# Performance work log

Hardware: AMD Instinct MI355X
Metric: run time of the kernel (lower is better)

The kernel has to match this reference:

```python
import jax, jax.numpy as jnp
import numpy as np

B, T, C = 2, 2048, 1024
H = 16
HD = C // H  # 64
BLOCK_SIZE = 2048
ROPE_BASE = 10000.0
NEG_INF = float('-inf')


def setup_inputs() -> dict:
    key = jax.random.key(0)
    k1, k2, k3, k4, k5, k6, k7 = jax.random.split(key, 7)
    x = jax.random.normal(k1, (B, T, C), dtype=jnp.float32)
    cumulative_scores = jax.random.normal(k2, (B, T), dtype=jnp.float32)
    padding_mask = jnp.ones((B, BLOCK_SIZE), dtype=jnp.bool_)
    token_index = jax.random.randint(k3, (B, T), 0, BLOCK_SIZE, dtype=jnp.int32)
    c_attn_weight = 0.02 * jax.random.normal(k4, (C, 3 * C), dtype=jnp.float32)
    c_attn_bias = jnp.zeros((3 * C,), dtype=jnp.float32)
    c_proj_weight = 0.02 * jax.random.normal(k5, (C, C), dtype=jnp.float32)
    c_proj_bias = jnp.zeros((C,), dtype=jnp.float32)
    return {
        'x': x,
        'cumulative_scores': cumulative_scores,
        'padding_mask': padding_mask,
        'token_index': token_index,
        'c_attn_weight': c_attn_weight,
        'c_attn_bias': c_attn_bias,
        'c_proj_weight': c_proj_weight,
        'c_proj_bias': c_proj_bias,
    }


def _rotate_half(x):
    x1, x2 = x[..., : x.shape[-1] // 2], x[..., x.shape[-1] // 2:]
    return jnp.concatenate((-x2, x1), axis=-1)


def _forward(x, cumulative_scores, c_attn_weight, c_attn_bias, c_proj_weight,
             c_proj_bias, token_index, padding_mask):
    # qkv projection
    qkv = x @ c_attn_weight + c_attn_bias
    q, k, v = jnp.split(qkv, 3, axis=2)
    q = q.reshape(B, T, H, HD).transpose(0, 2, 1, 3)  # [B,H,T,HD]
    k = k.reshape(B, T, H, HD).transpose(0, 2, 1, 3)
    v = v.reshape(B, T, H, HD).transpose(0, 2, 1, 3)

    # data-dependent per-token rotation amounts (faithful to source: the
    # scatter x.at[..., idx].add(1) with 2D idx accumulates over all batches)
    token_counts = jnp.zeros((B, BLOCK_SIZE), dtype=token_index.dtype)
    token_counts = token_counts.at[..., token_index].add(1)
    inv_counts = 1.0 / (token_counts + 1e-10)  # [B, BLOCK_SIZE] float32
    partial_rotations = jnp.cumsum(
        jnp.take_along_axis(inv_counts, token_index, axis=-1), axis=-1)  # [B,T]

    # RoPE with per-token t
    inv_freq = 1.0 / ROPE_BASE ** (jnp.arange(0, HD, 2, dtype=jnp.float32) / HD)
    freqs = jnp.einsum('bt,j->btj', partial_rotations, inv_freq)  # [B,T,HD/2]
    emb = jnp.concatenate((freqs, freqs), axis=-1)  # [B,T,HD]
    cos = jnp.cos(emb)[:, None, :, :]  # [B,1,T,HD]
    sin = jnp.sin(emb)[:, None, :, :]
    q = q * cos + _rotate_half(q) * sin
    k = k * cos + _rotate_half(k) * sin

    # fork plan: overwrite last channel of q with ones, of k with cum scores
    q = q.at[:, :, :, -1].set(1.0)
    k = k.at[:, :, :, -1].set(jnp.broadcast_to(cumulative_scores[:, None, :], (B, H, T)))

    # causal + padding additive mask
    causal = jnp.where(jnp.tril(jnp.ones((T, T), dtype=jnp.bool_)), 0.0, NEG_INF)  # [T,T]
    pm = jnp.take_along_axis(padding_mask, token_index, axis=1).astype(jnp.float32)  # [B,T]
    pm_outer = pm[:, :, None] * pm[:, None, :]  # [B,T,T]
    pm_add = jnp.where(pm_outer.astype(jnp.bool_), 0.0, NEG_INF)
    mask = causal[None, :, :] + pm_add  # [B,T,T]

    # v scaled by exp(cumulative_scores) along L
    v = v * jnp.exp(cumulative_scores)[:, None, :, None]

    scale = 1.0 / jnp.sqrt(jnp.asarray(HD, dtype=jnp.float32))
    attn = jnp.einsum('bnqd,bnkd->bnqk', q, k) * scale + mask[:, None, :, :]
    attn = jax.nn.softmax(attn, axis=-1)
    y = jnp.einsum('bnqk,bnkd->bnqd', attn, v)
    y = y.transpose(0, 2, 1, 3).reshape(B, T, C)
    return y @ c_proj_weight + c_proj_bias


def reference(x, cumulative_scores, padding_mask, token_index, c_attn_weight,
              c_attn_bias, c_proj_weight, c_proj_bias):
    return _forward(x, cumulative_scores, c_attn_weight, c_attn_bias,
                    c_proj_weight, c_proj_bias, token_index, padding_mask)
```

## Files before the change

### kernel.cpp

```cpp
#include <hip/hip_runtime.h>
#include <hip/hip_bf16.h>
#include <math.h>

#define Bb 2
#define Tt 2048
#define Cc 1024
#define Hh 16
#define HDd 64
#define QSCALE 0.18033688011112042f

typedef __attribute__((ext_vector_type(8))) short short8;
typedef __attribute__((ext_vector_type(4))) short short4v;
typedef __attribute__((ext_vector_type(4))) float f32x4;

#if defined(__has_builtin)
#if __has_builtin(__builtin_amdgcn_global_load_lds)
#define USE_GLL 1
#endif
#endif
#define AS_GLOBAL __attribute__((address_space(1)))
#define AS_LDS    __attribute__((address_space(3)))

__device__ __forceinline__ float bf2f(unsigned short u){
  union { unsigned int i; float f; } v; v.i = ((unsigned int)u)<<16; return v.f;
}
__device__ __forceinline__ unsigned short f2bf(float f){
  union { float f; unsigned int i; } v; v.f = f;
  unsigned int x = v.i;
  return (unsigned short)((x + 0x7fffu + ((x>>16)&1u)) >> 16);
}
__device__ __forceinline__ unsigned int cvtpk_bf16(float lo, float hi){
  unsigned int r;
  asm("v_cvt_pk_bf16_f32 %0, %1, %2" : "=v"(r) : "v"(lo), "v"(hi));
  return r;
}
__device__ __forceinline__ float exp2fast(float x){
  float r; asm("v_exp_f32 %0, %1" : "=v"(r) : "v"(x)); return r;
}
__device__ __forceinline__ f32x4 mfma16(short4v a, short4v b, f32x4 c){
#if defined(__has_builtin)
#if __has_builtin(__builtin_amdgcn_mfma_f32_16x16x16_bf16)
  return __builtin_amdgcn_mfma_f32_16x16x16_bf16(a, b, c, 0, 0, 0);
#elif __has_builtin(__builtin_amdgcn_mfma_f32_16x16x16bf16_1k)
  return __builtin_amdgcn_mfma_f32_16x16x16bf16_1k(a, b, c, 0, 0, 0);
#else
  asm("v_mfma_f32_16x16x16_bf16 %0, %1, %2, %3" : "=v"(c) : "v"(a), "v"(b), "0"(c));
  return c;
#endif
#else
  asm("v_mfma_f32_16x16x16_bf16 %0, %1, %2, %3" : "=v"(c) : "v"(a), "v"(b), "0"(c));
  return c;
#endif
}

__global__ __launch_bounds__(256) void k_f2b(const float* __restrict__ in,
                                             unsigned short* __restrict__ out, int n){
  int i = (blockIdx.x*256 + threadIdx.x)*8;
  if (i >= n) return;
  float4 v0 = *(const float4*)(in + i);
  float4 v1 = *(const float4*)(in + i + 4);
  union { unsigned int u[4]; int4 v; } pk;
  pk.u[0] = cvtpk_bf16(v0.x, v0.y);
  pk.u[1] = cvtpk_bf16(v0.z, v0.w);
  pk.u[2] = cvtpk_bf16(v1.x, v1.y);
  pk.u[3] = cvtpk_bf16(v1.z, v1.w);
  *(int4*)(out + i) = pk.v;
}

__global__ __launch_bounds__(256) void k_transpose_f2b(const float* __restrict__ w0,
                                                       const float* __restrict__ w1,
                                                       unsigned short* __restrict__ o0,
                                                       unsigned short* __restrict__ o1){
  __shared__ float tile[32][33];
  const int K = 1024;
  int which = blockIdx.z;
  const float* in = which ? w1 : w0;
  unsigned short* out = which ? o1 : o0;
  int N = which ? 1024 : 3072;
  if (blockIdx.x*32 >= N) return;
  int kb = blockIdx.y*32, nb = blockIdx.x*32;
  int tx = threadIdx.x, ty = threadIdx.y;
  #pragma unroll
  for (int i=0;i<4;i++)
    tile[ty+i*8][tx] = in[(size_t)(kb+ty+i*8)*N + nb + tx];
  __syncthreads();
  #pragma unroll
  for (int i=0;i<4;i++)
    out[(size_t)(nb+ty+i*8)*K + kb + tx] = f2bf(tile[tx][ty+i*8]);
}

__global__ __launch_bounds__(1024) void k_scan(const int* __restrict__ tok,
                                               float* __restrict__ cs_t){
  __shared__ int cnt[2048];
  __shared__ float vals[2048];
  __shared__ float psum[1024];
  int b = blockIdx.x;
  int tid = threadIdx.x;
  cnt[tid] = 0; cnt[tid+1024] = 0;
  __syncthreads();
  for (int i = tid; i < Bb*Tt; i += 1024) atomicAdd(&cnt[tok[i]], 1);
  __syncthreads();
  for (int i = tid; i < Tt; i += 1024){
    int idx = tok[b*Tt + i];
    vals[i] = 1.0f / ((float)cnt[idx] + 1e-10f);
  }
  __syncthreads();
  float s0 = vals[2*tid], s1 = vals[2*tid+1];
  psum[tid] = s0 + s1;
  __syncthreads();
  for (int off=1; off<1024; off<<=1){
    float add = (tid>=off) ? psum[tid-off] : 0.0f;
    __syncthreads();
    psum[tid] += add;
    __syncthreads();
  }
  float base = (tid>0) ? psum[tid-1] : 0.0f;
  vals[2*tid]   = base + s0;
  vals[2*tid+1] = base + s0 + s1;
  __syncthreads();
  for (int i = tid; i < Tt*32; i += 1024){
    int t = i >> 5, j = i & 31;
    float invf = exp2f(-(float)j * 0.4152410118609203f);
    float ang = vals[t] * invf;
    float2 cs = make_float2(cosf(ang), sinf(ang));
    *(float2*)&cs_t[((size_t)b*Tt + t)*64 + 2*j] = cs;
  }
}

__global__ __launch_bounds__(256, 4) void k_gemmQKV(const unsigned short* __restrict__ A,
                                                    const unsigned short* __restrict__ Bt,
                                                    const float* __restrict__ bias,
                                                    const float* __restrict__ cs_t,
                                                    const float* __restrict__ cum,
                                                    unsigned short* __restrict__ Qo,
                                                    unsigned short* __restrict__ Ko,
                                                    unsigned short* __restrict__ VTo){
  __shared__ union {
    unsigned short ab[2][128][64];
    unsigned short vb[32][140];
  } sm;
  const int K = 1024, N = 3072;
  int mb = blockIdx.y*128, nb = blockIdx.x*128;
  int tid = threadIdx.x;
  int wave = tid>>6, lane = tid&63;
  int wr = wave>>1, wc = wave&1;
  int lrow = lane&15, lhi = lane>>4;
  f32x4 acc[4][4] = {};
  int r0 = tid>>3;
  int g0 = tid&7;
  int gsw = (g0 ^ (r0&7)) << 3;
  const unsigned short* Asrc = A  + (size_t)(mb + r0)*K + gsw;
  const unsigned short* Bsrc = Bt + (size_t)(nb + r0)*K + gsw;
  const size_t rstep = (size_t)32*K;
#ifdef USE_GLL
  for (int kb=0; kb<K; kb+=64){
    #pragma unroll
    for (int i=0;i<4;i++){
      __builtin_amdgcn_global_load_lds((const AS_GLOBAL void*)(Asrc + i*rstep + kb),
                                       (AS_LDS void*)&sm.ab[0][r0+32*i][g0*8], 16, 0, 0);
      __builtin_amdgcn_global_load_lds((const AS_GLOBAL void*)(Bsrc + i*rstep + kb),
                                       (AS_LDS void*)&sm.ab[1][r0+32*i][g0*8], 16, 0, 0);
    }
    __syncthreads();
    #pragma unroll
    for (int ks=0; ks<2; ks++){
      short8 af[4], bf[4];
      #pragma unroll
      for (int m=0;m<4;m++){
        int R = 64*wr + 16*m + lrow;
        af[m] = *(const short8*)&sm.ab[0][R][((4*ks+lhi)^(R&7))<<3];
      }
      #pragma unroll
      for (int n=0;n<4;n++){
        int R = 64*wc + 16*n + lrow;
        bf[n] = *(const short8*)&sm.ab[1][R][((4*ks+lhi)^(R&7))<<3];
      }
      #pragma unroll
      for (int m=0;m<4;m++)
        #pragma unroll
        for (int n=0;n<4;n++)
          acc[m][n] = __builtin_amdgcn_mfma_f32_16x16x32_bf16(af[m], bf[n], acc[m][n], 0,0,0);
    }
    __syncthreads();
  }
#else
  for (int kb=0; kb<K; kb+=64){
    int4 st[8];
    #pragma unroll
    for (int i=0;i<4;i++){
      st[2*i]   = *(const int4*)(Asrc + i*rstep + kb);
      st[2*i+1] = *(const int4*)(Bsrc + i*rstep + kb);
    }
    __syncthreads();
    #pragma unroll
    for (int i=0;i<4;i++){
      *(int4*)&sm.ab[0][r0+32*i][g0*8] = st[2*i];
      *(int4*)&sm.ab[1][r0+32*i][g0*8] = st[2*i+1];
    }
    __syncthreads();
    #pragma unroll
    for (int ks=0; ks<2; ks++){
      short8 af[4], bf[4];
      #pragma unroll
      for (int m=0;m<4;m++){
        int R = 64*wr + 16*m + lrow;
        af[m] = *(const short8*)&sm.ab[0][R][((4*ks+lhi)^(R&7))<<3];
      }
      #pragma unroll
      for (int n=0;n<4;n++){
        int R = 64*wc + 16*n + lrow;
        bf[n] = *(const short8*)&sm.ab[1][R][((4*ks+lhi)^(R&7))<<3];
      }
      #pragma unroll
      for (int m=0;m<4;m++)
        #pragma unroll
        for (int n=0;n<4;n++)
          acc[m][n] = __builtin_amdgcn_mfma_f32_16x16x32_bf16(af[m], bf[n], acc[m][n], 0,0,0);
    }
    __syncthreads();
  }
#endif
  int type = nb >> 10;
  int h0 = (nb >> 6) & 15;
  int h  = h0 + wc;
  int b_ = mb >> 11;
  int tb_ = mb & 2047;
  float bz[4];
  #pragma unroll
  for (int n=0;n<4;n++) bz[n] = bias[nb + 64*wc + 16*n + lrow];

  if (type < 2){
    unsigned short* dst = (type==0) ? Qo : Ko;
    #pragma unroll
    for (int m=0;m<4;m++)
      #pragma unroll
      for (int q=0;q<4;q++){
        int rl = 64*wr + 16*m + 4*lhi + q;
        int row = mb + rl;
        float2 cs0 = *(const float2*)&cs_t[(size_t)row*64 + 2*lrow];
        float2 cs1 = *(const float2*)&cs_t[(size_t)row*64 + 32 + 2*lrow];
        float a0 = acc[m][0][q] + bz[0];
        float a1 = acc[m][1][q] + bz[1];
        float a2 = acc[m][2][q] + bz[2];
        float a3 = acc[m][3][q] + bz[3];
        float r0v = a0*cs0.x - a2*cs0.y;
        float r1v = a1*cs1.x - a3*cs1.y;
        float r2v = a2*cs0.x + a0*cs0.y;
        float r3v = a3*cs1.x + a1*cs1.y;
        if (type==0){
          if (lrow==15) r3v = 1.0f;
          r0v *= QSCALE; r1v *= QSCALE; r2v *= QSCALE; r3v *= QSCALE;
        } else {
          if (lrow==15) r3v = cum[row];
        }
        size_t base = (((size_t)b_*Hh + h)*Tt + (row & 2047))*HDd + lrow;
        dst[base]      = f2bf(r0v);
        dst[base + 16] = f2bf(r1v);
        dst[base + 32] = f2bf(r2v);
        dst[base + 48] = f2bf(r3v);
      }
  } else {
    for (int pass=0; pass<4; pass++){
      __syncthreads();
      if (wr == (pass>>1)){
        int m0 = 2*(pass&1);
        #pragma unroll
        for (int mm=0; mm<2; mm++){
          int m = m0 + mm;
          #pragma unroll
          for (int q=0;q<4;q++){
            int rl32 = 16*mm + 4*lhi + q;
            float vs = __expf(cum[mb + 32*pass + rl32]);
            sm.vb[rl32][64*wc + lrow]      = f2bf((acc[m][0][q]+bz[0])*vs);
            sm.vb[rl32][64*wc + 16+lrow]   = f2bf((acc[m][1][q]+bz[1])*vs);
            sm.vb[rl32][64*wc + 32+lrow]   = f2bf((acc[m][2][q]+bz[2])*vs);
            sm.vb[rl32][64*wc + 48+lrow]   = f2bf((acc[m][3][q]+bz[3])*vs);
          }
        }
      }
      __syncthreads();
      #pragma unroll
      for (int i=0;i<16;i++){
        int idx = i*256 + tid;
        int t_l = idx & 31;
        int dh  = idx >> 5;
        int d   = dh & 63;
        int hh  = dh >> 6;
        VTo[(((size_t)b_*Hh + h0 + hh)*HDd + d)*Tt + tb_ + 32*pass + t_l] = sm.vb[t_l][64*hh + d];
      }
    }
  }
}

__global__ __launch_bounds__(256) void k_gemm64(const unsigned short* __restrict__ A,
                                                const unsigned short* __restrict__ Bt,
                                                const float* __restrict__ bias,
                                                float* __restrict__ Cout,
                                                int M, int N, int K){
  __shared__ unsigned short As[64][32];
  __shared__ unsigned short Bs[128][32];
  int mb = blockIdx.y*64, nb = blockIdx.x*128;
  int tid = threadIdx.x;
  int wave = tid>>6, lane = tid&63;
  int wr = wave>>1, wc = wave&1;
  int lrow = lane&15, lhi = lane>>4;
  f32x4 acc[2][4] = {};
  int r0 = tid>>2;
  int gd = tid&3;
  int gs0 = (gd ^ ((r0>>1)&3)) << 3;
  const unsigned short* Arow  = A  + (size_t)(mb + r0)*K      + gs0;
  const unsigned short* Brow0 = Bt + (size_t)(nb + r0)*K      + gs0;
  const unsigned short* Brow1 = Bt + (size_t)(nb + r0 + 64)*K + gs0;
#ifdef USE_GLL
  for (int kb=0; kb<K; kb+=32){
    __builtin_amdgcn_global_load_lds((const AS_GLOBAL void*)(Arow + kb),
                                     (AS_LDS void*)&As[r0][gd*8],    16, 0, 0);
    __builtin_amdgcn_global_load_lds((const AS_GLOBAL void*)(Brow0 + kb),
                                     (AS_LDS void*)&Bs[r0][gd*8],    16, 0, 0);
    __builtin_amdgcn_global_load_lds((const AS_GLOBAL void*)(Brow1 + kb),
                                     (AS_LDS void*)&Bs[r0+64][gd*8], 16, 0, 0);
    __syncthreads();
    short8 af[2], bf[4];
    #pragma unroll
    for (int m=0;m<2;m++){
      int R = 32*wr + 16*m + lrow;
      af[m] = *(const short8*)&As[R][(lhi^((R>>1)&3))<<3];
    }
    #pragma unroll
    for (int n=0;n<4;n++){
      int R = 64*wc + 16*n + lrow;
      bf[n] = *(const short8*)&Bs[R][(lhi^((R>>1)&3))<<3];
    }
    #pragma unroll
    for (int m=0;m<2;m++)
      #pragma unroll
      for (int n=0;n<4;n++)
        acc[m][n] = __builtin_amdgcn_mfma_f32_16x16x32_bf16(af[m], bf[n], acc[m][n], 0,0,0);
    __syncthreads();
  }
#else
  for (int kb=0; kb<K; kb+=32){
    int4 a0 = *(const int4*)(Arow + kb);
    int4 b0 = *(const int4*)(Brow0 + kb);
    int4 b1 = *(const int4*)(Brow1 + kb);
    __syncthreads();
    *(int4*)&As[r0][gd*8]    = a0;
    *(int4*)&Bs[r0][gd*8]    = b0;
    *(int4*)&Bs[r0+64][gd*8] = b1;
    __syncthreads();
    short8 af[2], bf[4];
    #pragma unroll
    for (int m=0;m<2;m++){
      int R = 32*wr + 16*m + lrow;
      af[m] = *(const short8*)&As[R][(lhi^((R>>1)&3))<<3];
    }
    #pragma unroll
    for (int n=0;n<4;n++){
      int R = 64*wc + 16*n + lrow;
      bf[n] = *(const short8*)&Bs[R][(lhi^((R>>1)&3))<<3];
    }
    #pragma unroll
    for (int m=0;m<2;m++)
      #pragma unroll
      for (int n=0;n<4;n++)
        acc[m][n] = __builtin_amdgcn_mfma_f32_16x16x32_bf16(af[m], bf[n], acc[m][n], 0,0,0);
  }
#endif
  #pragma unroll
  for (int m=0;m<2;m++)
    #pragma unroll
    for (int n=0;n<4;n++)
      #pragma unroll
      for (int q=0;q<4;q++){
        int row = mb + 32*wr + 16*m + 4*lhi + q;
        int col = nb + 64*wc + 16*n + lrow;
        Cout[(size_t)row*N + col] = acc[m][n][q] + bias[col];
      }
}

__global__ __launch_bounds__(512, 4) void k_attn8(const unsigned short* __restrict__ Q,
                                                  const unsigned short* __restrict__ K,
                                                  const unsigned short* __restrict__ VT,
                                                  unsigned short* __restrict__ Y){
  __shared__ __align__(16) char smem[65536];
  typedef unsigned short (*tile_t)[2][4096];
  tile_t Ks = (tile_t)smem;
  tile_t Vs = (tile_t)(smem + 32768);
  float (*cmb)[64][35] = (float (*)[64][35])smem;

  int bh = blockIdx.y; int b = bh >> 4, h = bh & 15;
  int s_ = blockIdx.x;
  int tid = threadIdx.x;
  int wave = tid>>6, lane = tid&63;
  int wpair = wave & 3, p = wave >> 2;
  int lrow = lane&15, lhi = lane>>4;
  const unsigned short* Qh = Q + (((size_t)b*Hh + h)*Tt)*HDd;
  const unsigned short* Kh = K + (((size_t)b*Hh + h)*Tt)*HDd;
  const unsigned short* Vh = VT + (((size_t)b*Hh + h)*HDd)*Tt;
  int qL0 = 64*s_ + 16*wpair;
  int qH0 = 1984 - 64*s_ + 16*wpair;
  short8 qfL0 = *(const short8*)&Qh[(size_t)(qL0+lrow)*HDd + 8*lhi];
  short8 qfL1 = *(const short8*)&Qh[(size_t)(qL0+lrow)*HDd + 32 + 8*lhi];
  short8 qfH0 = *(const short8*)&Qh[(size_t)(qH0+lrow)*HDd + 8*lhi];
  short8 qfH1 = *(const short8*)&Qh[(size_t)(qH0+lrow)*HDd + 32 + 8*lhi];
  f32x4 oL[4] = {}, oH[4] = {};
  float lsL = 0.0f, lsH = 0.0f;
  int rowL = qL0 + lrow, rowH = qH0 + lrow;
  int ntL = s_ + 1;
  int NTH = 32 - s_;
  int NI  = (NTH + 1) >> 1;

  int kr = tid >> 3, kc = tid & 7;
  int o_ = tid * 16;
  int ksrc = kr*HDd + ((kc ^ (kr&7)) << 3);
  int vsrc = kr*Tt  + ((kc ^ (kr&7)) << 3);

#ifdef USE_GLL
#define STAGE2(bufi, base_) do { \
    __builtin_amdgcn_global_load_lds((const AS_GLOBAL void*)(Kh + (size_t)(base_)*64*HDd + ksrc), \
        (AS_LDS void*)((AS_LDS char*)&Ks[bufi][0][0] + o_), 16, 0, 0); \
    __builtin_amdgcn_global_load_lds((const AS_GLOBAL void*)(Vh + (size_t)(base_)*64 + vsrc), \
        (AS_LDS void*)((AS_LDS char*)&Vs[bufi][0][0] + o_), 16, 0, 0); \
    if ((base_)+1 < NTH){ \
      __builtin_amdgcn_global_load_lds((const AS_GLOBAL void*)(Kh + (size_t)((base_)+1)*64*HDd + ksrc), \
          (AS_LDS void*)((AS_LDS char*)&Ks[bufi][1][0] + o_), 16, 0, 0); \
      __builtin_amdgcn_global_load_lds((const AS_GLOBAL void*)(Vh + (size_t)((base_)+1)*64 + vsrc), \
          (AS_LDS void*)((AS_LDS char*)&Vs[bufi][1][0] + o_), 16, 0, 0); \
    } \
  } while(0)
#else
#define STAGE2(bufi, base_) do { \
    int4 a_ = *(const int4*)(Kh + (size_t)(base_)*64*HDd + ksrc); \
    int4 c_ = *(const int4*)(Vh + (size_t)(base_)*64 + vsrc); \
    *(int4*)((char*)&Ks[bufi][0][0] + o_) = a_; \
    *(int4*)((char*)&Vs[bufi][0][0] + o_) = c_; \
    if ((base_)+1 < NTH){ \
      int4 b_ = *(const int4*)(Kh + (size_t)((base_)+1)*64*HDd + ksrc); \
      int4 d_ = *(const int4*)(Vh + (size_t)((base_)+1)*64 + vsrc); \
      *(int4*)((char*)&Ks[bufi][1][0] + o_) = b_; \
      *(int4*)((char*)&Vs[bufi][1][0] + o_) = d_; \
    } \
  } while(0)
#endif

  STAGE2(0, 0);
  int buf = 0;
  for (int i = 0; i < NI; i++){
    __syncthreads();
    if (i+1 < NI) STAGE2(buf^1, 2*(i+1));
    int kt = 2*i + p;
    if (kt < NTH){
      int k0 = kt*64;
      bool doL = (kt < ntL);
      const unsigned short* Kbase = &Ks[buf][p][0];
      const unsigned short* Vbase = &Vs[buf][p][0];
      f32x4 sL[4] = {}, sH[4] = {};
      __builtin_amdgcn_s_setprio(1);
      #pragma unroll
      for (int j=0;j<4;j++){
        int krow = 16*j + lrow;
        #pragma unroll
        for (int ks=0;ks<2;ks++){
          int dgrp = (4*ks + lhi) ^ (krow&7);
          short8 kf = *(const short8*)&Kbase[krow*64 + dgrp*8];
          sH[j] = __builtin_amdgcn_mfma_f32_16x16x32_bf16(kf, ks ? qfH1 : qfH0, sH[j], 0,0,0);
          if (doL) sL[j] = __builtin_amdgcn_mfma_f32_16x16x32_bf16(kf, ks ? qfL1 : qfL0, sL[j], 0,0,0);
        }
      }
      __builtin_amdgcn_s_setprio(0);
      short4v paH[4], paL[4];
      {
        bool diagH = (k0 + 63 >= qH0);
        #pragma unroll
        for (int j=0;j<4;j++){
          int kbase = k0 + 16*j + 4*lhi;
          float p0 = exp2fast(sH[j][0]);
          float p1 = exp2fast(sH[j][1]);
          float p2 = exp2fast(sH[j][2]);
          float p3 = exp2fast(sH[j][3]);
          if (diagH){
            if (kbase + 0 > rowH) p0 = 0.0f;
            if (kbase + 1 > rowH) p1 = 0.0f;
            if (kbase + 2 > rowH) p2 = 0.0f;
            if (kbase + 3 > rowH) p3 = 0.0f;
          }
          lsH += (p0 + p1) + (p2 + p3);
          union { unsigned int u[2]; short4v v; } pk;
          pk.u[0] = cvtpk_bf16(p0, p1);
          pk.u[1] = cvtpk_bf16(p2, p3);
          paH[j] = pk.v;
        }
      }
      if (doL){
        bool diagL = (k0 + 63 >= qL0);
        #pragma unroll
        for (int j=0;j<4;j++){
          int kbase = k0 + 16*j + 4*lhi;
          float p0 = exp2fast(sL[j][0]);
          float p1 = exp2fast(sL[j][1]);
          float p2 = exp2fast(sL[j][2]);
          float p3 = exp2fast(sL[j][3]);
          if (diagL){
            if (kbase + 0 > rowL) p0 = 0.0f;
            if (kbase + 1 > rowL) p1 = 0.0f;
            if (kbase + 2 > rowL) p2 = 0.0f;
            if (kbase + 3 > rowL) p3 = 0.0f;
          }
          lsL += (p0 + p1) + (p2 + p3);
          union { unsigned int u[2]; short4v v; } pk;
          pk.u[0] = cvtpk_bf16(p0, p1);
          pk.u[1] = cvtpk_bf16(p2, p3);
          paL[j] = pk.v;
        }
      }
      __builtin_amdgcn_s_setprio(1);
      #pragma unroll
      for (int jp=0;jp<4;jp++){
        int vrow = 16*jp + lrow;
        #pragma unroll
        for (int j=0;j<4;j++){
          int byte_in_row = ((((2*j + (lhi>>1)) ^ (vrow&7)) << 4) | ((lhi&1) << 3));
          short4v vf = *(const short4v*)((const char*)&Vbase[vrow*64] + byte_in_row);
          oH[jp] = mfma16(vf, paH[j], oH[jp]);
          if (doL) oL[jp] = mfma16(vf, paL[j], oL[jp]);
        }
      }
      __builtin_amdgcn_s_setprio(0);
    }
    buf ^= 1;
  }

  __syncthreads();
  if (p == 1){
    float* c = &cmb[wpair][lane][0];
    #pragma unroll
    for (int jp=0;jp<4;jp++)
      #pragma unroll
      for (int r=0;r<4;r++){
        c[4*jp+r]    = oL[jp][r];
        c[16+4*jp+r] = oH[jp][r];
      }
    c[32] = lsL; c[33] = lsH;
  }
  __syncthreads();
  if (p == 0){
    const float* c = &cmb[wpair][lane][0];
    #pragma unroll
    for (int jp=0;jp<4;jp++)
      #pragma unroll
      for (int r=0;r<4;r++){
        oL[jp][r] += c[4*jp+r];
        oH[jp][r] += c[16+4*jp+r];
      }
    lsL += c[32]; lsH += c[33];
    lsL += __shfl_xor(lsL, 16); lsL += __shfl_xor(lsL, 32);
    lsH += __shfl_xor(lsH, 16); lsH += __shfl_xor(lsH, 32);
    float invL = 1.0f / lsL, invH = 1.0f / lsH;
    size_t rbL = ((size_t)b*Tt + qL0 + lrow)*Cc + h*HDd + 4*lhi;
    size_t rbH = ((size_t)b*Tt + qH0 + lrow)*Cc + h*HDd + 4*lhi;
    #pragma unroll
    for (int jp=0;jp<4;jp++){
      unsigned int l0 = cvtpk_bf16(oL[jp][0]*invL, oL[jp][1]*invL);
      unsigned int l1 = cvtpk_bf16(oL[jp][2]*invL, oL[jp][3]*invL);
      unsigned int h0_ = cvtpk_bf16(oH[jp][0]*invH, oH[jp][1]*invH);
      unsigned int h1_ = cvtpk_bf16(oH[jp][2]*invH, oH[jp][3]*invH);
      *(unsigned long long*)&Y[rbL + 16*jp] = (unsigned long long)l0 | ((unsigned long long)l1<<32);
      *(unsigned long long*)&Y[rbH + 16*jp] = (unsigned long long)h0_ | ((unsigned long long)h1_<<32);
    }
  }
#undef STAGE2
}

extern "C" void kernel_launch(void* const* d_in, const int* in_sizes, int n_in,
                              void* d_out, int out_size, void* d_ws, size_t ws_size,
                              hipStream_t stream){
  const float* x     = (const float*)d_in[0];
  const float* cum   = (const float*)d_in[1];
  const int*   tok   = (const int*)d_in[3];
  const float* Wqkv  = (const float*)d_in[4];
  const float* bqkv  = (const float*)d_in[5];
  const float* Wproj = (const float*)d_in[6];
  const float* bproj = (const float*)d_in[7];

  char* ws = (char*)d_ws;
  size_t off = 0;
  auto alloc = [&](size_t bytes)->void*{
    void* p = ws + off; off += (bytes + 255) & ~(size_t)255; return p;
  };
  unsigned short* wqkvT = (unsigned short*)alloc((size_t)3072*1024*2);
  unsigned short* wprojT= (unsigned short*)alloc((size_t)1024*1024*2);
  unsigned short* xb    = (unsigned short*)alloc((size_t)4096*1024*2);
  unsigned short* Qb    = (unsigned short*)alloc((size_t)Bb*Hh*Tt*HDd*2);
  unsigned short* Kb    = (unsigned short*)alloc((size_t)Bb*Hh*Tt*HDd*2);
  unsigned short* VTb   = (unsigned short*)alloc((size_t)Bb*Hh*Tt*HDd*2);
  float* cs_t           = (float*)alloc((size_t)Bb*Tt*64*4);
  unsigned short* Y     = xb;

  k_f2b<<<dim3(4096*1024/8/256), dim3(256), 0, stream>>>(x, xb, 4096*1024);
  k_transpose_f2b<<<dim3(3072/32, 1024/32, 2), dim3(32,8), 0, stream>>>(Wqkv, Wproj, wqkvT, wprojT);
  k_scan<<<dim3(Bb), dim3(1024), 0, stream>>>(tok, cs_t);
  k_gemmQKV<<<dim3(3072/128, 4096/128), dim3(256), 0, stream>>>(xb, wqkvT, bqkv, cs_t, cum, Qb, Kb, VTb);
  k_attn8<<<dim3(16, Bb*Hh), dim3(512), 0, stream>>>(Qb, Kb, VTb, Y);
  k_gemm64<<<dim3(1024/128, 4096/64), dim3(256), 0, stream>>>(Y, wprojT, bproj, (float*)d_out, 4096, 1024, 1024);
}
```

Baseline: 133.7 us.

## Fuse fp32-to-bf16 conversion of x into the QKV GEMM A-tile load

Removes the separate k_f2b conversion kernel and has the QKV GEMM load fp32 activations straight into LDS with an XOR swizzle, converting to bf16 when building the MFMA fragments. This saves one launch plus a full write and read of the bf16 copy of x. In exchange the A tile in LDS doubles in size (fp32), which may lower occupancy, and the conversion is repeated by every N-column block. It also raises wave priority around the MFMA loop with s_setprio.

```diff
diff --git a/kernel.cpp b/kernel.cpp
--- a/kernel.cpp
+++ b/kernel.cpp
@@ -51,20 +51,6 @@
   asm("v_mfma_f32_16x16x16_bf16 %0, %1, %2, %3" : "=v"(c) : "v"(a), "v"(b), "0"(c));
   return c;
 #endif
-}
-
-__global__ __launch_bounds__(256) void k_f2b(const float* __restrict__ in,
-                                             unsigned short* __restrict__ out, int n){
-  int i = (blockIdx.x*256 + threadIdx.x)*8;
-  if (i >= n) return;
-  float4 v0 = *(const float4*)(in + i);
-  float4 v1 = *(const float4*)(in + i + 4);
-  union { unsigned int u[4]; int4 v; } pk;
-  pk.u[0] = cvtpk_bf16(v0.x, v0.y);
-  pk.u[1] = cvtpk_bf16(v0.z, v0.w);
-  pk.u[2] = cvtpk_bf16(v1.x, v1.y);
-  pk.u[3] = cvtpk_bf16(v1.z, v1.w);
-  *(int4*)(out + i) = pk.v;
 }
 
 __global__ __launch_bounds__(256) void k_transpose_f2b(const float* __restrict__ w0,
@@ -127,7 +113,7 @@
   }
 }
 
-__global__ __launch_bounds__(256, 4) void k_gemmQKV(const unsigned short* __restrict__ A,
+__global__ __launch_bounds__(256, 4) void k_gemmQKV(const float* __restrict__ A,
                                                     const unsigned short* __restrict__ Bt,
                                                     const float* __restrict__ bias,
                                                     const float* __restrict__ cs_t,
@@ -136,7 +122,10 @@
                                                     unsigned short* __restrict__ Ko,
                                                     unsigned short* __restrict__ VTo){
   __shared__ union {
-    unsigned short ab[2][128][64];
+    struct {
+      float          Af[128][64];
+      unsigned short Bs[128][64];
+    } s;
     unsigned short vb[32][140];
   } sm;
   const int K = 1024, N = 3072;
@@ -146,20 +135,26 @@
   int wr = wave>>1, wc = wave&1;
   int lrow = lane&15, lhi = lane>>4;
   f32x4 acc[4][4] = {};
-  int r0 = tid>>3;
-  int g0 = tid&7;
-  int gsw = (g0 ^ (r0&7)) << 3;
-  const unsigned short* Asrc = A  + (size_t)(mb + r0)*K + gsw;
-  const unsigned short* Bsrc = Bt + (size_t)(nb + r0)*K + gsw;
-  const size_t rstep = (size_t)32*K;
+  int r0b = tid>>3, g0 = tid&7;
+  int gswB = (g0 ^ (r0b&7)) << 3;
+  const unsigned short* Bsrc = Bt + (size_t)(nb + r0b)*K + gswB;
+  const size_t rstepB = (size_t)32*K;
+  int ar = tid>>1;
 #ifdef USE_GLL
   for (int kb=0; kb<K; kb+=64){
     #pragma unroll
+    for (int i=0;i<8;i++){
+      int flat = i*256 + tid;
+      int r = flat >> 4, g = flat & 15;
+      __builtin_amdgcn_global_load_lds(
+        (const AS_GLOBAL void*)(A + (size_t)(mb + r)*K + kb + ((g ^ (r&7)) << 2)),
+        (AS_LDS void*)&sm.s.Af[r][g<<2], 16, 0, 0);
+    }
+    #pragma unroll
     for (int i=0;i<4;i++){
-      __builtin_amdgcn_global_load_lds((const AS_GLOBAL void*)(Asrc + i*rstep + kb),
-                                       (AS_LDS void*)&sm.ab[0][r0+32*i][g0*8], 16, 0, 0);
-      __builtin_amdgcn_global_load_lds((const AS_GLOBAL void*)(Bsrc + i*rstep + kb),
-                                       (AS_LDS void*)&sm.ab[1][r0+32*i][g0*8], 16, 0, 0);
+      __builtin_amdgcn_global_load_lds(
+        (const AS_GLOBAL void*)(Bsrc + i*rstepB + kb),
+        (AS_LDS void*)&sm.s.Bs[r0b+32*i][g0*8], 16, 0, 0);
     }
     __syncthreads();
     #pragma unroll
@@ -168,35 +163,51 @@
       #pragma unroll
       for (int m=0;m<4;m++){
         int R = 64*wr + 16*m + lrow;
-        af[m] = *(const short8*)&sm.ab[0][R][((4*ks+lhi)^(R&7))<<3];
+        int G0 = 8*ks + 2*lhi;
+        f32x4 a0 = *(const f32x4*)&sm.s.Af[R][(G0     ^ (R&7)) << 2];
+        f32x4 a1 = *(const f32x4*)&sm.s.Af[R][((G0+1) ^ (R&7)) << 2];
+        union { unsigned int u[4]; short8 v; } pa;
+        pa.u[0] = cvtpk_bf16(a0[0], a0[1]);
+        pa.u[1] = cvtpk_bf16(a0[2], a0[3]);
+        pa.u[2] = cvtpk_bf16(a1[0], a1[1]);
+        pa.u[3] = cvtpk_bf16(a1[2], a1[3]);
+        af[m] = pa.v;
       }
       #pragma unroll
       for (int n=0;n<4;n++){
         int R = 64*wc + 16*n + lrow;
-        bf[n] = *(const short8*)&sm.ab[1][R][((4*ks+lhi)^(R&7))<<3];
-      }
+        bf[n] = *(const short8*)&sm.s.Bs[R][((4*ks+lhi)^(R&7))<<3];
+      }
+      __builtin_amdgcn_s_setprio(1);
       #pragma unroll
       for (int m=0;m<4;m++)
         #pragma unroll
         for (int n=0;n<4;n++)
           acc[m][n] = __builtin_amdgcn_mfma_f32_16x16x32_bf16(af[m], bf[n], acc[m][n], 0,0,0);
+      __builtin_amdgcn_s_setprio(0);
     }
     __syncthreads();
   }
 #else
   for (int kb=0; kb<K; kb+=64){
-    int4 st[8];
-    #pragma unroll
-    for (int i=0;i<4;i++){
-      st[2*i]   = *(const int4*)(Asrc + i*rstep + kb);
-      st[2*i+1] = *(const int4*)(Bsrc + i*rstep + kb);
-    }
-    __syncthreads();
-    #pragma unroll
-    for (int i=0;i<4;i++){
-      *(int4*)&sm.ab[0][r0+32*i][g0*8] = st[2*i];
-      *(int4*)&sm.ab[1][r0+32*i][g0*8] = st[2*i+1];
-    }
+    float4 sa[8]; int4 sb[4];
+    #pragma unroll
+    for (int i=0;i<8;i++){
+      int flat = i*256 + tid;
+      int r = flat >> 4, g = flat & 15;
+      sa[i] = *(const float4*)(A + (size_t)(mb + r)*K + kb + ((g ^ (r&7)) << 2));
+    }
+    #pragma unroll
+    for (int i=0;i<4;i++) sb[i] = *(const int4*)(Bsrc + i*rstepB + kb);
+    __syncthreads();
+    #pragma unroll
+    for (int i=0;i<8;i++){
+      int flat = i*256 + tid;
+      int r = flat >> 4, g = flat & 15;
+      *(float4*)&sm.s.Af[r][g<<2] = sa[i];
+    }
+    #pragma unroll
+    for (int i=0;i<4;i++) *(int4*)&sm.s.Bs[r0b+32*i][g0*8] = sb[i];
     __syncthreads();
     #pragma unroll
     for (int ks=0; ks<2; ks++){
@@ -204,12 +215,20 @@
       #pragma unroll
       for (int m=0;m<4;m++){
         int R = 64*wr + 16*m + lrow;
-        af[m] = *(const short8*)&sm.ab[0][R][((4*ks+lhi)^(R&7))<<3];
+        int G0 = 8*ks + 2*lhi;
+        f32x4 a0 = *(const f32x4*)&sm.s.Af[R][(G0     ^ (R&7)) << 2];
+        f32x4 a1 = *(const f32x4*)&sm.s.Af[R][((G0+1) ^ (R&7)) << 2];
+        union { unsigned int u[4]; short8 v; } pa;
+        pa.u[0] = cvtpk_bf16(a0[0], a0[1]);
+        pa.u[1] = cvtpk_bf16(a0[2], a0[3]);
+        pa.u[2] = cvtpk_bf16(a1[0], a1[1]);
+        pa.u[3] = cvtpk_bf16(a1[2], a1[3]);
+        af[m] = pa.v;
       }
       #pragma unroll
       for (int n=0;n<4;n++){
         int R = 64*wc + 16*n + lrow;
-        bf[n] = *(const short8*)&sm.ab[1][R][((4*ks+lhi)^(R&7))<<3];
+        bf[n] = *(const short8*)&sm.s.Bs[R][((4*ks+lhi)^(R&7))<<3];
       }
       #pragma unroll
       for (int m=0;m<4;m++)
@@ -589,17 +608,15 @@
   };
   unsigned short* wqkvT = (unsigned short*)alloc((size_t)3072*1024*2);
   unsigned short* wprojT= (unsigned short*)alloc((size_t)1024*1024*2);
-  unsigned short* xb    = (unsigned short*)alloc((size_t)4096*1024*2);
+  unsigned short* Y     = (unsigned short*)alloc((size_t)4096*1024*2);
   unsigned short* Qb    = (unsigned short*)alloc((size_t)Bb*Hh*Tt*HDd*2);
   unsigned short* Kb    = (unsigned short*)alloc((size_t)Bb*Hh*Tt*HDd*2);
   unsigned short* VTb   = (unsigned short*)alloc((size_t)Bb*Hh*Tt*HDd*2);
   float* cs_t           = (float*)alloc((size_t)Bb*Tt*64*4);
-  unsigned short* Y     = xb;
-
-  k_f2b<<<dim3(4096*1024/8/256), dim3(256), 0, stream>>>(x, xb, 4096*1024);
+
   k_transpose_f2b<<<dim3(3072/32, 1024/32, 2), dim3(32,8), 0, stream>>>(Wqkv, Wproj, wqkvT, wprojT);
   k_scan<<<dim3(Bb), dim3(1024), 0, stream>>>(tok, cs_t);
-  k_gemmQKV<<<dim3(3072/128, 4096/128), dim3(256), 0, stream>>>(xb, wqkvT, bqkv, cs_t, cum, Qb, Kb, VTb);
+  k_gemmQKV<<<dim3(3072/128, 4096/128), dim3(256), 0, stream>>>(x, wqkvT, bqkv, cs_t, cum, Qb, Kb, VTb);
   k_attn8<<<dim3(16, Bb*Hh), dim3(512), 0, stream>>>(Qb, Kb, VTb, Y);
   k_gemm64<<<dim3(1024/128, 4096/64), dim3(256), 0, stream>>>(Y, wprojT, bproj, (float*)d_out, 4096, 1024, 1024);
 }
```

Result: slower. 190.4 us (+42.5%).
